# Performance work log

Measured on AMD Instinct MI355X. Metric: run time of the kernel, lower is better.

## Reference

```python
import jax, jax.numpy as jnp
import numpy as np

N_NODES = 100000
N_EDGES = 1600000
NFEAT, NHID, NCLASS = 128, 64, 40
NLAYERS = 4
P = 2.0


def setup_inputs() -> dict:
    key = jax.random.key(0)
    ks = jax.random.split(key, 10)
    x = jax.random.normal(ks[0], (N_NODES, NFEAT), dtype=jnp.float32)
    edge_index = jax.random.randint(ks[1], (2, N_EDGES), 0, N_NODES, dtype=jnp.int32)
    s_in = 1.0 / np.sqrt(NFEAT)
    s_h = 1.0 / np.sqrt(NHID)
    return {
        "x": x,
        "edge_index": edge_index,
        "enc_W": jax.random.normal(ks[2], (NHID, NFEAT), dtype=jnp.float32) * s_in,
        "enc_b": jnp.zeros((NHID,), dtype=jnp.float32),
        "conv_W": jax.random.normal(ks[3], (NHID, NHID), dtype=jnp.float32) * s_h,
        "conv_b": jnp.zeros((NHID,), dtype=jnp.float32),
        "W_skip": jax.random.normal(ks[4], (NHID, NHID), dtype=jnp.float32) * s_h,
        "dec_W": jax.random.normal(ks[5], (NCLASS, NHID), dtype=jnp.float32) * s_h,
        "dec_b": jnp.zeros((NCLASS,), dtype=jnp.float32),
    }


def _gcn_conv(X, W, b, src, dst, n):
    # PyG GCNConv: add self-loops, symmetric normalization, then X @ W^T + b
    H = X @ W.T  # [n, nhid]
    ones = jnp.ones_like(dst, dtype=X.dtype)
    deg = jax.ops.segment_sum(ones, dst, num_segments=n)  # in-degree incl. self loops
    dinv = jnp.where(deg > 0, jax.lax.rsqrt(deg), 0.0)
    norm = dinv[src] * dinv[dst]  # [E+n]
    out = jax.ops.segment_sum(norm[:, None] * H[src], dst, num_segments=n)
    return out + b


def _gamma(X, row, col, n, p):
    # G2 gating: scatter-mean over edges of sum |X[row]-X[col]|^p, then tanh.
    # (conv_gg output in the original G2 is dead code and omitted.)
    diff = jnp.sum(jnp.abs(X[row] - X[col]) ** p, axis=-1)  # [E]
    s = jax.ops.segment_sum(diff, row, num_segments=n)
    cnt = jax.ops.segment_sum(jnp.ones_like(diff), row, num_segments=n)
    return jnp.tanh(s / jnp.maximum(cnt, 1.0))  # [n]


def reference(x, edge_index, enc_W, enc_b, conv_W, conv_b, W_skip, dec_W, dec_b):
    n = x.shape[0]
    row, col = edge_index[0], edge_index[1]
    # self-loop augmented edges for GCNConv
    loop = jnp.arange(n, dtype=edge_index.dtype)
    src_sl = jnp.concatenate([row, loop])
    dst_sl = jnp.concatenate([col, loop])

    X = jax.nn.relu(x @ enc_W.T + enc_b)  # [n, nhid]
    X_init = X
    skip_val = X_init @ W_skip.T  # constant across layers

    for _ in range(NLAYERS):
        X_agg = jax.nn.relu(_gcn_conv(X, conv_W, conv_b, src_sl, dst_sl, n))
        g = _gamma(X, row, col, n, P)[:, None]  # gamma_smooth == gamma_squash (dead convs)
        denom = 1.0 + g + g
        A = 1.0 / denom
        B = g / denom
        C = g / denom
        X = A * X + B * X_agg + C * skip_val

    return X @ dec_W.T + dec_b  # [n, nclass]
```

## Files before the change

### kernel.cpp

```cpp
#include <hip/hip_runtime.h>
#include <hip/hip_bf16.h>

#define NFEAT 128
#define NHID  64
#define NCLASS 40
#define NLAYERS 4


__global__ void count_edges_k(const int* __restrict__ ei, int E,
                              int* __restrict__ cnt_row, int* __restrict__ cnt_col,
                              int* __restrict__ rank) {
    int e = blockIdx.x * blockDim.x + threadIdx.x;
    if (e >= E) return;
    int r = ei[e];
    int c = ei[E + e];
    atomicAdd(&cnt_row[r], 1);
    rank[e] = atomicAdd(&cnt_col[c], 1);
}

__global__ void dinv_k(const int* __restrict__ cnt_col, float* __restrict__ dinv, int n) {
    int v = blockIdx.x * blockDim.x + threadIdx.x;
    if (v >= n) return;
    dinv[v] = 1.0f / sqrtf((float)(cnt_col[v] + 1));
}

__global__ void scanA_k(const int* __restrict__ cnt, int* __restrict__ off,
                        int* __restrict__ bsum, int n) {
    __shared__ int t[1024];
    int i = blockIdx.x * 1024 + threadIdx.x;
    int x = (i < n) ? cnt[i] : 0;
    t[threadIdx.x] = x;
    __syncthreads();
    for (int d = 1; d < 1024; d <<= 1) {
        int y = (threadIdx.x >= (unsigned)d) ? t[threadIdx.x - d] : 0;
        __syncthreads();
        t[threadIdx.x] += y;
        __syncthreads();
    }
    if (i < n) off[i] = t[threadIdx.x] - x;
    if (threadIdx.x == 1023) bsum[blockIdx.x] = t[1023];
}

__global__ void scanB_k(int* __restrict__ bsum, int nb) {
    __shared__ int t[1024];
    int x = (threadIdx.x < (unsigned)nb) ? bsum[threadIdx.x] : 0;
    t[threadIdx.x] = x;
    __syncthreads();
    for (int d = 1; d < 1024; d <<= 1) {
        int y = (threadIdx.x >= (unsigned)d) ? t[threadIdx.x - d] : 0;
        __syncthreads();
        t[threadIdx.x] += y;
        __syncthreads();
    }
    if (threadIdx.x < (unsigned)nb) bsum[threadIdx.x] = t[threadIdx.x] - x;
}

__global__ void scanC_k(int* __restrict__ off, const int* __restrict__ bsum, int n, int total) {
    int i = blockIdx.x * 1024 + threadIdx.x;
    if (i < n) off[i] += bsum[blockIdx.x];
    if (i == 0) off[n] = total;
}

__global__ void fill_k(const int* __restrict__ ei, int E, const float* __restrict__ dinv,
                       const int* __restrict__ col_off, const int* __restrict__ rank,
                       uint2* __restrict__ csr) {
    int e = blockIdx.x * blockDim.x + threadIdx.x;
    if (e >= E) return;
    int r = ei[e];
    int c = ei[E + e];
    uint2 ent;
    ent.x = (unsigned)r;
    ent.y = __float_as_uint(dinv[r]);
    csr[col_off[c] + rank[e]] = ent;
}


template<int K, int M, bool RELU, bool BIAS>
__global__ void dense_k(const float* __restrict__ A, const float* __restrict__ W,
                        const float* __restrict__ b, float* __restrict__ out, int n) {
    int v = blockIdx.x * blockDim.x + threadIdx.x;
    if (v >= n) return;
    float a[K];
    const float4* ap = reinterpret_cast<const float4*>(A + (size_t)v * K);
#pragma unroll
    for (int k = 0; k < K / 4; ++k) {
        float4 t = ap[k];
        a[4 * k + 0] = t.x; a[4 * k + 1] = t.y; a[4 * k + 2] = t.z; a[4 * k + 3] = t.w;
    }
    float4* op = reinterpret_cast<float4*>(out + (size_t)v * M);
#pragma unroll 1
    for (int m = 0; m < M; m += 4) {
        float acc0 = BIAS ? b[m + 0] : 0.f;
        float acc1 = BIAS ? b[m + 1] : 0.f;
        float acc2 = BIAS ? b[m + 2] : 0.f;
        float acc3 = BIAS ? b[m + 3] : 0.f;
#pragma unroll
        for (int k = 0; k < K; ++k) {
            float av = a[k];
            acc0 = fmaf(av, W[(m + 0) * K + k], acc0);
            acc1 = fmaf(av, W[(m + 1) * K + k], acc1);
            acc2 = fmaf(av, W[(m + 2) * K + k], acc2);
            acc3 = fmaf(av, W[(m + 3) * K + k], acc3);
        }
        if (RELU) {
            acc0 = fmaxf(acc0, 0.f); acc1 = fmaxf(acc1, 0.f);
            acc2 = fmaxf(acc2, 0.f); acc3 = fmaxf(acc3, 0.f);
        }
        float4 o; o.x = acc0; o.y = acc1; o.z = acc2; o.w = acc3;
        op[m >> 2] = o;
    }
}

__global__ void gather_k(const float* __restrict__ X, const uint2* __restrict__ csr,
                         const int* __restrict__ col_off, const float* __restrict__ dinv,
                         float* __restrict__ pre, float* __restrict__ gs, int n) {
    int v = blockIdx.x * 4 + (threadIdx.x >> 6);
    if (v >= n) return;
    int lane = threadIdx.x & 63;
    int grp = lane >> 4;
    int sub = lane & 15;

    float4 xv = reinterpret_cast<const float4*>(X + (size_t)v * NHID)[sub];
    int beg = col_off[v], end = col_off[v + 1];

    float4 acc = make_float4(0.f, 0.f, 0.f, 0.f);
    for (int e = beg + grp; e < end; e += 4) {
        uint2 ent = csr[e];
        float4 xs = reinterpret_cast<const float4*>(X + (size_t)ent.x * NHID)[sub];
        float w = __uint_as_float(ent.y);
        acc.x = fmaf(w, xs.x, acc.x);
        acc.y = fmaf(w, xs.y, acc.y);
        acc.z = fmaf(w, xs.z, acc.z);
        acc.w = fmaf(w, xs.w, acc.w);
        float dx = xs.x - xv.x;
        float part = dx * dx;
        dx = xs.y - xv.y; part = fmaf(dx, dx, part);
        dx = xs.z - xv.z; part = fmaf(dx, dx, part);
        dx = xs.w - xv.w; part = fmaf(dx, dx, part);
#pragma unroll
        for (int m = 1; m <= 8; m <<= 1) part += __shfl_xor(part, m, 64);
        if (sub == 0) atomicAdd(&gs[ent.x], part);
    }
#pragma unroll
    for (int m = 16; m <= 32; m <<= 1) {
        acc.x += __shfl_xor(acc.x, m, 64);
        acc.y += __shfl_xor(acc.y, m, 64);
        acc.z += __shfl_xor(acc.z, m, 64);
        acc.w += __shfl_xor(acc.w, m, 64);
    }
    if (grp == 0) {
        float dv = dinv[v];
        float dv2 = dv * dv;
        float4 o;
        o.x = fmaf(dv, acc.x, dv2 * xv.x);
        o.y = fmaf(dv, acc.y, dv2 * xv.y);
        o.z = fmaf(dv, acc.z, dv2 * xv.z);
        o.w = fmaf(dv, acc.w, dv2 * xv.w);
        reinterpret_cast<float4*>(pre + (size_t)v * NHID)[sub] = o;
    }
}

__global__ void update_k(float* __restrict__ X, const float* __restrict__ pre,
                         const float* __restrict__ skip, const float* __restrict__ W,
                         const float* __restrict__ b, float* __restrict__ gs,
                         const int* __restrict__ cnt_row, int n) {
    int v = blockIdx.x * blockDim.x + threadIdx.x;
    if (v >= n) return;
    float a[NHID];
    const float4* ap = reinterpret_cast<const float4*>(pre + (size_t)v * NHID);
#pragma unroll
    for (int k = 0; k < NHID / 4; ++k) {
        float4 t = ap[k];
        a[4 * k + 0] = t.x; a[4 * k + 1] = t.y; a[4 * k + 2] = t.z; a[4 * k + 3] = t.w;
    }
    float gv = tanhf(gs[v] / fmaxf((float)cnt_row[v], 1.f));
    gs[v] = 0.f;
    float inv = 1.0f / (1.0f + 2.0f * gv);

    float4* Xp = reinterpret_cast<float4*>(X + (size_t)v * NHID);
    const float4* Sp = reinterpret_cast<const float4*>(skip + (size_t)v * NHID);
#pragma unroll 1
    for (int m = 0; m < NHID; m += 4) {
        float t0 = b[m + 0], t1 = b[m + 1], t2 = b[m + 2], t3 = b[m + 3];
#pragma unroll
        for (int k = 0; k < NHID; ++k) {
            float av = a[k];
            t0 = fmaf(av, W[(m + 0) * NHID + k], t0);
            t1 = fmaf(av, W[(m + 1) * NHID + k], t1);
            t2 = fmaf(av, W[(m + 2) * NHID + k], t2);
            t3 = fmaf(av, W[(m + 3) * NHID + k], t3);
        }
        t0 = fmaxf(t0, 0.f); t1 = fmaxf(t1, 0.f);
        t2 = fmaxf(t2, 0.f); t3 = fmaxf(t3, 0.f);
        float4 x4 = Xp[m >> 2];
        float4 s4 = Sp[m >> 2];
        float4 o;
        o.x = (x4.x + gv * (t0 + s4.x)) * inv;
        o.y = (x4.y + gv * (t1 + s4.y)) * inv;
        o.z = (x4.z + gv * (t2 + s4.z)) * inv;
        o.w = (x4.w + gv * (t3 + s4.w)) * inv;
        Xp[m >> 2] = o;
    }
}


extern "C" void kernel_launch(void* const* d_in, const int* in_sizes, int n_in,
                              void* d_out, int out_size, void* d_ws, size_t ws_size,
                              hipStream_t stream) {
    const float* x      = (const float*)d_in[0];
    const int*   ei     = (const int*)  d_in[1];
    const float* enc_W  = (const float*)d_in[2];
    const float* enc_b  = (const float*)d_in[3];
    const float* conv_W = (const float*)d_in[4];
    const float* conv_b = (const float*)d_in[5];
    const float* W_skip = (const float*)d_in[6];
    const float* dec_W  = (const float*)d_in[7];
    const float* dec_b  = (const float*)d_in[8];

    const int n = in_sizes[0] / NFEAT;
    const int E = in_sizes[1] / 2;

    char* ws = (char*)d_ws;
    auto alloc = [&](size_t bytes) {
        char* p = ws;
        ws += (bytes + 255) & ~(size_t)255;
        return p;
    };

    float* X    = (float*)alloc((size_t)n * NHID * 4);
    float* pre  = (float*)alloc((size_t)n * NHID * 4);
    float* skip = (float*)alloc((size_t)n * NHID * 4);
    float* gs   = (float*)alloc((size_t)n * 4);
    float* dinv = (float*)alloc((size_t)n * 4);
    int* cnt_row = (int*)alloc((size_t)n * 4);
    int* cnt_col = (int*)alloc((size_t)n * 4);
    int* col_off = (int*)alloc((size_t)(n + 1) * 4);
    int* rank    = (int*)alloc((size_t)E * 4);
    int* bsc     = (int*)alloc(1024 * 4);
    uint2* csr   = (uint2*)alloc((size_t)E * 8);

    hipMemsetAsync(cnt_row, 0, (size_t)n * 4, stream);
    hipMemsetAsync(cnt_col, 0, (size_t)n * 4, stream);
    hipMemsetAsync(gs, 0, (size_t)n * 4, stream);

    count_edges_k<<<(E + 255) / 256, 256, 0, stream>>>(ei, E, cnt_row, cnt_col, rank);
    dinv_k<<<(n + 255) / 256, 256, 0, stream>>>(cnt_col, dinv, n);

    int nb = (n + 1023) / 1024;
    scanA_k<<<nb, 1024, 0, stream>>>(cnt_col, col_off, bsc, n);
    scanB_k<<<1, 1024, 0, stream>>>(bsc, nb);
    scanC_k<<<nb, 1024, 0, stream>>>(col_off, bsc, n, E);
    fill_k<<<(E + 255) / 256, 256, 0, stream>>>(ei, E, dinv, col_off, rank, csr);

    dense_k<NFEAT, NHID, true, true><<<(n + 255) / 256, 256, 0, stream>>>(x, enc_W, enc_b, X, n);
    dense_k<NHID, NHID, false, false><<<(n + 255) / 256, 256, 0, stream>>>(X, W_skip, nullptr, skip, n);

    for (int l = 0; l < NLAYERS; ++l) {
        gather_k<<<(n + 3) / 4, 256, 0, stream>>>(X, csr, col_off, dinv, pre, gs, n);
        update_k<<<(n + 255) / 256, 256, 0, stream>>>(X, pre, skip, conv_W, conv_b, gs, cnt_row, n);
    }

    dense_k<NHID, NCLASS, false, true><<<(n + 255) / 256, 256, 0, stream>>>(X, dec_W, dec_b, (float*)d_out, n);
}
```

Baseline: 942.9 us.

## Compact CSR to source indices, fill via atomic cursors, restructure dense matvecs

The CSR build drops the per-edge rank array. It fills slots with atomic cursors seeded from the column offsets, and stores only the source index (4 bytes instead of 8). The gather now looks up dinv per edge instead of reading it packed alongside the index. The dense and update kernels are reordered to stream the input in float4 chunks while keeping all outputs in accumulator registers, which raises register pressure but avoids reloading the input row. The goal is less CSR traffic in the four gather passes and cheaper setup; the trade-off is an extra dinv gather per edge and possible occupancy loss from the larger register footprint.

```diff
diff --git a/kernel.cpp b/kernel.cpp
--- a/kernel.cpp
+++ b/kernel.cpp
@@ -8,14 +8,11 @@
 
 
 __global__ void count_edges_k(const int* __restrict__ ei, int E,
-                              int* __restrict__ cnt_row, int* __restrict__ cnt_col,
-                              int* __restrict__ rank) {
+                              int* __restrict__ cnt_row, int* __restrict__ cnt_col) {
     int e = blockIdx.x * blockDim.x + threadIdx.x;
     if (e >= E) return;
-    int r = ei[e];
-    int c = ei[E + e];
-    atomicAdd(&cnt_row[r], 1);
-    rank[e] = atomicAdd(&cnt_col[c], 1);
+    atomicAdd(&cnt_row[ei[e]], 1);
+    atomicAdd(&cnt_col[ei[E + e]], 1);
 }
 
 __global__ void dinv_k(const int* __restrict__ cnt_col, float* __restrict__ dinv, int n) {
@@ -55,23 +52,39 @@
     if (threadIdx.x < (unsigned)nb) bsum[threadIdx.x] = t[threadIdx.x] - x;
 }
 
-__global__ void scanC_k(int* __restrict__ off, const int* __restrict__ bsum, int n, int total) {
+__global__ void scanC_k(int* __restrict__ off, const int* __restrict__ bsum,
+                        int* __restrict__ cur, int n, int total) {
     int i = blockIdx.x * 1024 + threadIdx.x;
-    if (i < n) off[i] += bsum[blockIdx.x];
+    if (i < n) {
+        int o = off[i] + bsum[blockIdx.x];
+        off[i] = o;
+        cur[i] = o;
+    }
     if (i == 0) off[n] = total;
 }
 
-__global__ void fill_k(const int* __restrict__ ei, int E, const float* __restrict__ dinv,
-                       const int* __restrict__ col_off, const int* __restrict__ rank,
-                       uint2* __restrict__ csr) {
-    int e = blockIdx.x * blockDim.x + threadIdx.x;
-    if (e >= E) return;
-    int r = ei[e];
-    int c = ei[E + e];
-    uint2 ent;
-    ent.x = (unsigned)r;
-    ent.y = __float_as_uint(dinv[r]);
-    csr[col_off[c] + rank[e]] = ent;
+__global__ void fill_k(const int* __restrict__ ei, int E,
+                       int* __restrict__ cur, int* __restrict__ csr) {
+    int t = blockIdx.x * blockDim.x + threadIdx.x;
+    int base = t * 4;
+    if (base >= E) return;
+    if (base + 4 <= E) {
+        int4 r4 = *reinterpret_cast<const int4*>(ei + base);
+        int4 c4 = *reinterpret_cast<const int4*>(ei + E + base);
+        int p0 = atomicAdd(&cur[c4.x], 1);
+        int p1 = atomicAdd(&cur[c4.y], 1);
+        int p2 = atomicAdd(&cur[c4.z], 1);
+        int p3 = atomicAdd(&cur[c4.w], 1);
+        csr[p0] = r4.x;
+        csr[p1] = r4.y;
+        csr[p2] = r4.z;
+        csr[p3] = r4.w;
+    } else {
+        for (int e = base; e < E; ++e) {
+            int p = atomicAdd(&cur[ei[E + e]], 1);
+            csr[p] = ei[e];
+        }
+    }
 }
 
 
@@ -80,38 +93,35 @@
                         const float* __restrict__ b, float* __restrict__ out, int n) {
     int v = blockIdx.x * blockDim.x + threadIdx.x;
     if (v >= n) return;
-    float a[K];
+    float acc[M];
+#pragma unroll
+    for (int m = 0; m < M; ++m) acc[m] = BIAS ? b[m] : 0.f;
     const float4* ap = reinterpret_cast<const float4*>(A + (size_t)v * K);
-#pragma unroll
-    for (int k = 0; k < K / 4; ++k) {
-        float4 t = ap[k];
-        a[4 * k + 0] = t.x; a[4 * k + 1] = t.y; a[4 * k + 2] = t.z; a[4 * k + 3] = t.w;
+#pragma unroll 1
+    for (int kb = 0; kb < K / 4; ++kb) {
+        float4 a4 = ap[kb];
+#pragma unroll
+        for (int m = 0; m < M; ++m) {
+            const float* wr = W + (size_t)m * K + kb * 4;
+            acc[m] = fmaf(a4.x, wr[0], acc[m]);
+            acc[m] = fmaf(a4.y, wr[1], acc[m]);
+            acc[m] = fmaf(a4.z, wr[2], acc[m]);
+            acc[m] = fmaf(a4.w, wr[3], acc[m]);
+        }
     }
     float4* op = reinterpret_cast<float4*>(out + (size_t)v * M);
-#pragma unroll 1
+#pragma unroll
     for (int m = 0; m < M; m += 4) {
-        float acc0 = BIAS ? b[m + 0] : 0.f;
-        float acc1 = BIAS ? b[m + 1] : 0.f;
-        float acc2 = BIAS ? b[m + 2] : 0.f;
-        float acc3 = BIAS ? b[m + 3] : 0.f;
-#pragma unroll
-        for (int k = 0; k < K; ++k) {
-            float av = a[k];
-            acc0 = fmaf(av, W[(m + 0) * K + k], acc0);
-            acc1 = fmaf(av, W[(m + 1) * K + k], acc1);
-            acc2 = fmaf(av, W[(m + 2) * K + k], acc2);
-            acc3 = fmaf(av, W[(m + 3) * K + k], acc3);
-        }
-        if (RELU) {
-            acc0 = fmaxf(acc0, 0.f); acc1 = fmaxf(acc1, 0.f);
-            acc2 = fmaxf(acc2, 0.f); acc3 = fmaxf(acc3, 0.f);
-        }
-        float4 o; o.x = acc0; o.y = acc1; o.z = acc2; o.w = acc3;
+        float4 o;
+        o.x = RELU ? fmaxf(acc[m + 0], 0.f) : acc[m + 0];
+        o.y = RELU ? fmaxf(acc[m + 1], 0.f) : acc[m + 1];
+        o.z = RELU ? fmaxf(acc[m + 2], 0.f) : acc[m + 2];
+        o.w = RELU ? fmaxf(acc[m + 3], 0.f) : acc[m + 3];
         op[m >> 2] = o;
     }
 }
 
-__global__ void gather_k(const float* __restrict__ X, const uint2* __restrict__ csr,
+__global__ void gather_k(const float* __restrict__ X, const int* __restrict__ csr,
                          const int* __restrict__ col_off, const float* __restrict__ dinv,
                          float* __restrict__ pre, float* __restrict__ gs, int n) {
     int v = blockIdx.x * 4 + (threadIdx.x >> 6);
@@ -125,9 +135,9 @@
 
     float4 acc = make_float4(0.f, 0.f, 0.f, 0.f);
     for (int e = beg + grp; e < end; e += 4) {
-        uint2 ent = csr[e];
-        float4 xs = reinterpret_cast<const float4*>(X + (size_t)ent.x * NHID)[sub];
-        float w = __uint_as_float(ent.y);
+        int s = csr[e];
+        float w = dinv[s];
+        float4 xs = reinterpret_cast<const float4*>(X + (size_t)s * NHID)[sub];
         acc.x = fmaf(w, xs.x, acc.x);
         acc.y = fmaf(w, xs.y, acc.y);
         acc.z = fmaf(w, xs.z, acc.z);
@@ -139,7 +149,7 @@
         dx = xs.w - xv.w; part = fmaf(dx, dx, part);
 #pragma unroll
         for (int m = 1; m <= 8; m <<= 1) part += __shfl_xor(part, m, 64);
-        if (sub == 0) atomicAdd(&gs[ent.x], part);
+        if (sub == 0) atomicAdd(&gs[s], part);
     }
 #pragma unroll
     for (int m = 16; m <= 32; m <<= 1) {
@@ -166,12 +176,21 @@
                          const int* __restrict__ cnt_row, int n) {
     int v = blockIdx.x * blockDim.x + threadIdx.x;
     if (v >= n) return;
-    float a[NHID];
+    float acc[NHID];
+#pragma unroll
+    for (int m = 0; m < NHID; ++m) acc[m] = b[m];
     const float4* ap = reinterpret_cast<const float4*>(pre + (size_t)v * NHID);
-#pragma unroll
-    for (int k = 0; k < NHID / 4; ++k) {
-        float4 t = ap[k];
-        a[4 * k + 0] = t.x; a[4 * k + 1] = t.y; a[4 * k + 2] = t.z; a[4 * k + 3] = t.w;
+#pragma unroll 1
+    for (int kb = 0; kb < NHID / 4; ++kb) {
+        float4 a4 = ap[kb];
+#pragma unroll
+        for (int m = 0; m < NHID; ++m) {
+            const float* wr = W + (size_t)m * NHID + kb * 4;
+            acc[m] = fmaf(a4.x, wr[0], acc[m]);
+            acc[m] = fmaf(a4.y, wr[1], acc[m]);
+            acc[m] = fmaf(a4.z, wr[2], acc[m]);
+            acc[m] = fmaf(a4.w, wr[3], acc[m]);
+        }
     }
     float gv = tanhf(gs[v] / fmaxf((float)cnt_row[v], 1.f));
     gs[v] = 0.f;
@@ -179,19 +198,12 @@
 
     float4* Xp = reinterpret_cast<float4*>(X + (size_t)v * NHID);
     const float4* Sp = reinterpret_cast<const float4*>(skip + (size_t)v * NHID);
-#pragma unroll 1
+#pragma unroll
     for (int m = 0; m < NHID; m += 4) {
-        float t0 = b[m + 0], t1 = b[m + 1], t2 = b[m + 2], t3 = b[m + 3];
-#pragma unroll
-        for (int k = 0; k < NHID; ++k) {
-            float av = a[k];
-            t0 = fmaf(av, W[(m + 0) * NHID + k], t0);
-            t1 = fmaf(av, W[(m + 1) * NHID + k], t1);
-            t2 = fmaf(av, W[(m + 2) * NHID + k], t2);
-            t3 = fmaf(av, W[(m + 3) * NHID + k], t3);
-        }
-        t0 = fmaxf(t0, 0.f); t1 = fmaxf(t1, 0.f);
-        t2 = fmaxf(t2, 0.f); t3 = fmaxf(t3, 0.f);
+        float t0 = fmaxf(acc[m + 0], 0.f);
+        float t1 = fmaxf(acc[m + 1], 0.f);
+        float t2 = fmaxf(acc[m + 2], 0.f);
+        float t3 = fmaxf(acc[m + 3], 0.f);
         float4 x4 = Xp[m >> 2];
         float4 s4 = Sp[m >> 2];
         float4 o;
@@ -235,22 +247,22 @@
     int* cnt_row = (int*)alloc((size_t)n * 4);
     int* cnt_col = (int*)alloc((size_t)n * 4);
     int* col_off = (int*)alloc((size_t)(n + 1) * 4);
-    int* rank    = (int*)alloc((size_t)E * 4);
+    int* cur     = (int*)alloc((size_t)n * 4);
     int* bsc     = (int*)alloc(1024 * 4);
-    uint2* csr   = (uint2*)alloc((size_t)E * 8);
+    int* csr     = (int*)alloc((size_t)E * 4);
 
     hipMemsetAsync(cnt_row, 0, (size_t)n * 4, stream);
     hipMemsetAsync(cnt_col, 0, (size_t)n * 4, stream);
     hipMemsetAsync(gs, 0, (size_t)n * 4, stream);
 
-    count_edges_k<<<(E + 255) / 256, 256, 0, stream>>>(ei, E, cnt_row, cnt_col, rank);
+    count_edges_k<<<(E + 255) / 256, 256, 0, stream>>>(ei, E, cnt_row, cnt_col);
     dinv_k<<<(n + 255) / 256, 256, 0, stream>>>(cnt_col, dinv, n);
 
     int nb = (n + 1023) / 1024;
     scanA_k<<<nb, 1024, 0, stream>>>(cnt_col, col_off, bsc, n);
     scanB_k<<<1, 1024, 0, stream>>>(bsc, nb);
-    scanC_k<<<nb, 1024, 0, stream>>>(col_off, bsc, n, E);
-    fill_k<<<(E + 255) / 256, 256, 0, stream>>>(ei, E, dinv, col_off, rank, csr);
+    scanC_k<<<nb, 1024, 0, stream>>>(col_off, bsc, cur, n, E);
+    fill_k<<<(E / 4 + 255) / 256, 256, 0, stream>>>(ei, E, cur, csr);
 
     dense_k<NFEAT, NHID, true, true><<<(n + 255) / 256, 256, 0, stream>>>(x, enc_W, enc_b, X, n);
     dense_k<NHID, NHID, false, false><<<(n + 255) / 256, 256, 0, stream>>>(X, W_skip, nullptr, skip, n);
```

New measurement: 1.228 ms. 30.3% more time.

## Shrink CSR to source indices and build it with cursor atomics

Applied to the files above, without the earlier changes.

Drops the per-edge rank array and builds the CSR with an atomic cursor per destination. The out-degree count moves into the fill pass, and both passes read edges four or eight at a time with vector loads. CSR entries shrink from (src, dinv) pairs to bare source indices, so the gather now looks up dinv[src], an extra dependent load that trades for less CSR traffic. The encoder matmul gets a dedicated kernel that streams the input in float4 chunks with 32 outputs per chunk, to ease register pressure. Neighbour order within a CSR segment is now nondeterministic, which can change floating-point summation order.

```diff
diff --git a/kernel.cpp b/kernel.cpp
--- a/kernel.cpp
+++ b/kernel.cpp
@@ -7,15 +7,19 @@
 #define NLAYERS 4
 
 
-__global__ void count_edges_k(const int* __restrict__ ei, int E,
-                              int* __restrict__ cnt_row, int* __restrict__ cnt_col,
-                              int* __restrict__ rank) {
-    int e = blockIdx.x * blockDim.x + threadIdx.x;
-    if (e >= E) return;
-    int r = ei[e];
-    int c = ei[E + e];
-    atomicAdd(&cnt_row[r], 1);
-    rank[e] = atomicAdd(&cnt_col[c], 1);
+__global__ void count_in_k(const int* __restrict__ ei, int E, int* __restrict__ cnt_col) {
+    int t = blockIdx.x * blockDim.x + threadIdx.x;
+    int base = t * 4;
+    if (base >= E) return;
+    if (base + 4 <= E) {
+        int4 c4 = *reinterpret_cast<const int4*>(ei + E + base);
+        atomicAdd(&cnt_col[c4.x], 1);
+        atomicAdd(&cnt_col[c4.y], 1);
+        atomicAdd(&cnt_col[c4.z], 1);
+        atomicAdd(&cnt_col[c4.w], 1);
+    } else {
+        for (int e = base; e < E; ++e) atomicAdd(&cnt_col[ei[E + e]], 1);
+    }
 }
 
 __global__ void dinv_k(const int* __restrict__ cnt_col, float* __restrict__ dinv, int n) {
@@ -55,29 +59,66 @@
     if (threadIdx.x < (unsigned)nb) bsum[threadIdx.x] = t[threadIdx.x] - x;
 }
 
-__global__ void scanC_k(int* __restrict__ off, const int* __restrict__ bsum, int n, int total) {
+__global__ void scanC_k(int* __restrict__ off, const int* __restrict__ bsum,
+                        int* __restrict__ cur, int n, int total) {
     int i = blockIdx.x * 1024 + threadIdx.x;
-    if (i < n) off[i] += bsum[blockIdx.x];
+    if (i < n) {
+        int o = off[i] + bsum[blockIdx.x];
+        off[i] = o;
+        cur[i] = o;
+    }
     if (i == 0) off[n] = total;
 }
 
-__global__ void fill_k(const int* __restrict__ ei, int E, const float* __restrict__ dinv,
-                       const int* __restrict__ col_off, const int* __restrict__ rank,
-                       uint2* __restrict__ csr) {
-    int e = blockIdx.x * blockDim.x + threadIdx.x;
-    if (e >= E) return;
-    int r = ei[e];
-    int c = ei[E + e];
-    uint2 ent;
-    ent.x = (unsigned)r;
-    ent.y = __float_as_uint(dinv[r]);
-    csr[col_off[c] + rank[e]] = ent;
+__global__ void fill_k(const int* __restrict__ ei, int E,
+                       int* __restrict__ cur, int* __restrict__ cnt_row,
+                       int* __restrict__ csr) {
+    int t = blockIdx.x * blockDim.x + threadIdx.x;
+    int base = t * 8;
+    if (base >= E) return;
+    if (base + 8 <= E) {
+        int4 rA = *reinterpret_cast<const int4*>(ei + base);
+        int4 rB = *reinterpret_cast<const int4*>(ei + base + 4);
+        int4 cA = *reinterpret_cast<const int4*>(ei + E + base);
+        int4 cB = *reinterpret_cast<const int4*>(ei + E + base + 4);
+        int p0 = atomicAdd(&cur[cA.x], 1);
+        int p1 = atomicAdd(&cur[cA.y], 1);
+        int p2 = atomicAdd(&cur[cA.z], 1);
+        int p3 = atomicAdd(&cur[cA.w], 1);
+        int p4 = atomicAdd(&cur[cB.x], 1);
+        int p5 = atomicAdd(&cur[cB.y], 1);
+        int p6 = atomicAdd(&cur[cB.z], 1);
+        int p7 = atomicAdd(&cur[cB.w], 1);
+        atomicAdd(&cnt_row[rA.x], 1);
+        atomicAdd(&cnt_row[rA.y], 1);
+        atomicAdd(&cnt_row[rA.z], 1);
+        atomicAdd(&cnt_row[rA.w], 1);
+        atomicAdd(&cnt_row[rB.x], 1);
+        atomicAdd(&cnt_row[rB.y], 1);
+        atomicAdd(&cnt_row[rB.z], 1);
+        atomicAdd(&cnt_row[rB.w], 1);
+        csr[p0] = rA.x;
+        csr[p1] = rA.y;
+        csr[p2] = rA.z;
+        csr[p3] = rA.w;
+        csr[p4] = rB.x;
+        csr[p5] = rB.y;
+        csr[p6] = rB.z;
+        csr[p7] = rB.w;
+    } else {
+        for (int e = base; e < E; ++e) {
+            int r = ei[e];
+            int p = atomicAdd(&cur[ei[E + e]], 1);
+            atomicAdd(&cnt_row[r], 1);
+            csr[p] = r;
+        }
+    }
 }
 
 
 template<int K, int M, bool RELU, bool BIAS>
-__global__ void dense_k(const float* __restrict__ A, const float* __restrict__ W,
-                        const float* __restrict__ b, float* __restrict__ out, int n) {
+__global__ void dense_small_k(const float* __restrict__ A, const float* __restrict__ W,
+                              const float* __restrict__ b, float* __restrict__ out, int n) {
     int v = blockIdx.x * blockDim.x + threadIdx.x;
     if (v >= n) return;
     float a[K];
@@ -111,7 +152,44 @@
     }
 }
 
-__global__ void gather_k(const float* __restrict__ X, const uint2* __restrict__ csr,
+
+template<int K, int M, int MC>
+__global__ void dense_enc_k(const float* __restrict__ A, const float* __restrict__ W,
+                            const float* __restrict__ b, float* __restrict__ out, int n) {
+    int v = blockIdx.x * blockDim.x + threadIdx.x;
+    if (v >= n) return;
+    const float4* ap = reinterpret_cast<const float4*>(A + (size_t)v * K);
+    float4* op = reinterpret_cast<float4*>(out + (size_t)v * M);
+#pragma unroll 1
+    for (int mc = 0; mc < M; mc += MC) {
+        float acc[MC];
+#pragma unroll
+        for (int m = 0; m < MC; ++m) acc[m] = b[mc + m];
+#pragma unroll 1
+        for (int kb = 0; kb < K / 4; ++kb) {
+            float4 a4 = ap[kb];
+#pragma unroll
+            for (int m = 0; m < MC; ++m) {
+                const float* wr = W + (size_t)(mc + m) * K + kb * 4;
+                acc[m] = fmaf(a4.x, wr[0], acc[m]);
+                acc[m] = fmaf(a4.y, wr[1], acc[m]);
+                acc[m] = fmaf(a4.z, wr[2], acc[m]);
+                acc[m] = fmaf(a4.w, wr[3], acc[m]);
+            }
+        }
+#pragma unroll
+        for (int m = 0; m < MC; m += 4) {
+            float4 o;
+            o.x = fmaxf(acc[m + 0], 0.f);
+            o.y = fmaxf(acc[m + 1], 0.f);
+            o.z = fmaxf(acc[m + 2], 0.f);
+            o.w = fmaxf(acc[m + 3], 0.f);
+            op[(mc + m) >> 2] = o;
+        }
+    }
+}
+
+__global__ void gather_k(const float* __restrict__ X, const int* __restrict__ csr,
                          const int* __restrict__ col_off, const float* __restrict__ dinv,
                          float* __restrict__ pre, float* __restrict__ gs, int n) {
     int v = blockIdx.x * 4 + (threadIdx.x >> 6);
@@ -125,9 +203,9 @@
 
     float4 acc = make_float4(0.f, 0.f, 0.f, 0.f);
     for (int e = beg + grp; e < end; e += 4) {
-        uint2 ent = csr[e];
-        float4 xs = reinterpret_cast<const float4*>(X + (size_t)ent.x * NHID)[sub];
-        float w = __uint_as_float(ent.y);
+        int s = csr[e];
+        float w = dinv[s];
+        float4 xs = reinterpret_cast<const float4*>(X + (size_t)s * NHID)[sub];
         acc.x = fmaf(w, xs.x, acc.x);
         acc.y = fmaf(w, xs.y, acc.y);
         acc.z = fmaf(w, xs.z, acc.z);
@@ -139,7 +217,7 @@
         dx = xs.w - xv.w; part = fmaf(dx, dx, part);
 #pragma unroll
         for (int m = 1; m <= 8; m <<= 1) part += __shfl_xor(part, m, 64);
-        if (sub == 0) atomicAdd(&gs[ent.x], part);
+        if (sub == 0) atomicAdd(&gs[s], part);
     }
 #pragma unroll
     for (int m = 16; m <= 32; m <<= 1) {
@@ -235,30 +313,30 @@
     int* cnt_row = (int*)alloc((size_t)n * 4);
     int* cnt_col = (int*)alloc((size_t)n * 4);
     int* col_off = (int*)alloc((size_t)(n + 1) * 4);
-    int* rank    = (int*)alloc((size_t)E * 4);
+    int* cur     = (int*)alloc((size_t)n * 4);
     int* bsc     = (int*)alloc(1024 * 4);
-    uint2* csr   = (uint2*)alloc((size_t)E * 8);
+    int* csr     = (int*)alloc((size_t)E * 4);
 
     hipMemsetAsync(cnt_row, 0, (size_t)n * 4, stream);
     hipMemsetAsync(cnt_col, 0, (size_t)n * 4, stream);
     hipMemsetAsync(gs, 0, (size_t)n * 4, stream);
 
-    count_edges_k<<<(E + 255) / 256, 256, 0, stream>>>(ei, E, cnt_row, cnt_col, rank);
+    count_in_k<<<(E / 4 + 255) / 256, 256, 0, stream>>>(ei, E, cnt_col);
     dinv_k<<<(n + 255) / 256, 256, 0, stream>>>(cnt_col, dinv, n);
 
     int nb = (n + 1023) / 1024;
     scanA_k<<<nb, 1024, 0, stream>>>(cnt_col, col_off, bsc, n);
     scanB_k<<<1, 1024, 0, stream>>>(bsc, nb);
-    scanC_k<<<nb, 1024, 0, stream>>>(col_off, bsc, n, E);
-    fill_k<<<(E + 255) / 256, 256, 0, stream>>>(ei, E, dinv, col_off, rank, csr);
-
-    dense_k<NFEAT, NHID, true, true><<<(n + 255) / 256, 256, 0, stream>>>(x, enc_W, enc_b, X, n);
-    dense_k<NHID, NHID, false, false><<<(n + 255) / 256, 256, 0, stream>>>(X, W_skip, nullptr, skip, n);
+    scanC_k<<<nb, 1024, 0, stream>>>(col_off, bsc, cur, n, E);
+    fill_k<<<(E / 8 + 255) / 256, 256, 0, stream>>>(ei, E, cur, cnt_row, csr);
+
+    dense_enc_k<NFEAT, NHID, 32><<<(n + 255) / 256, 256, 0, stream>>>(x, enc_W, enc_b, X, n);
+    dense_small_k<NHID, NHID, false, false><<<(n + 255) / 256, 256, 0, stream>>>(X, W_skip, nullptr, skip, n);
 
     for (int l = 0; l < NLAYERS; ++l) {
         gather_k<<<(n + 3) / 4, 256, 0, stream>>>(X, csr, col_off, dinv, pre, gs, n);
         update_k<<<(n + 255) / 256, 256, 0, stream>>>(X, pre, skip, conv_W, conv_b, gs, cnt_row, n);
     }
 
-    dense_k<NHID, NCLASS, false, true><<<(n + 255) / 256, 256, 0, stream>>>(X, dec_W, dec_b, (float*)d_out, n);
-}
+    dense_small_k<NHID, NCLASS, false, true><<<(n + 255) / 256, 256, 0, stream>>>(X, dec_W, dec_b, (float*)d_out, n);
+}
```

Result: slower. 1.052 ms (+11.5%).
